# Kernel optimization log

Hardware: AMD Instinct MI355X
Metric: run time of the kernel (lower is better)

Reference implementation:

```python
import jax, jax.numpy as jnp
import numpy as np

# nuScenes-scale config: batch 2, 360x360 BEV grid (1440/4), 128 channels,
# 10 classes, 200 proposals, 3x3 NMS kernel, 40k occupied voxels per sample.
B, H, W_GRID, NUM_CLS, NUM_PROP, NMS_K = 2, 360, 360, 10, 200, 3
C = 128
N_PER_B = 40000
NEG_FILL = -1000000.0  # scatter_nd fill value from to_dense()


def _bev_pos():
    # replicates create_2D_grid: coord = (x_index_along_dim1, y_index_along_dim0)
    xs = jnp.arange(H, dtype=jnp.float32)
    ys = jnp.arange(W_GRID, dtype=jnp.float32)
    by, bx = jnp.meshgrid(xs, ys, indexing='ij')  # by[i,j]=i, bx[i,j]=j
    return jnp.stack([bx, by], axis=-1).reshape(-1, 2)  # [H*W, 2]


def setup_inputs() -> dict:
    key = jax.random.key(0)
    ks = jax.random.split(key, 10)
    # unique spatial locations per batch sample (sparse voxel coords)
    flats = [jax.random.permutation(ks[i], H * W_GRID)[:N_PER_B] for i in range(B)]
    flat = jnp.concatenate(flats)
    b = jnp.repeat(jnp.arange(B), N_PER_B)
    indices = jnp.stack([b, flat // W_GRID, flat % W_GRID], axis=1).astype(jnp.int32)
    features = jax.random.normal(ks[4], (B * N_PER_B, C), jnp.float32)
    # heatmap head (pointwise linears standing in for the submconv stack)
    W_hm1 = jax.random.normal(ks[5], (C, C), jnp.float32) * (2.0 / C) ** 0.5
    b_hm1 = jnp.zeros((C,), jnp.float32)
    W_hm2 = jax.random.normal(ks[6], (C, NUM_CLS), jnp.float32) * (2.0 / C) ** 0.5
    b_hm2 = jnp.full((NUM_CLS,), -2.19, jnp.float32)  # fc[-1].bias.fill_(-2.19)
    # class_encoding: nn.Conv1d(num_class, channels, 1)
    W_cls = jax.random.normal(ks[7], (C, NUM_CLS), jnp.float32) * 0.1
    b_cls = jnp.zeros((C,), jnp.float32)
    return dict(features=features, W_hm1=W_hm1, b_hm1=b_hm1, W_hm2=W_hm2,
                b_hm2=b_hm2, W_cls=W_cls, b_cls=b_cls, indices=indices)


def reference(features, W_hm1, b_hm1, W_hm2, b_hm2, W_cls, b_cls, indices):
    bidx, yi, xi = indices[:, 0], indices[:, 1], indices[:, 2]
    HW = H * W_GRID

    # --- x.dense(): scatter voxel features to dense BEV grid (zero fill) ---
    xd = jnp.zeros((B, H, W_GRID, C), features.dtype).at[bidx, yi, xi].set(features)
    x_flat = xd.reshape(B, HW, C).transpose(0, 2, 1)  # [B, C, HW]

    # --- heatmap head (per-voxel) then to_dense() with -1e6 fill ---
    hm = jax.nn.relu(features @ W_hm1 + b_hm1) @ W_hm2 + b_hm2  # [N, NUM_CLS]
    dense_hm = jnp.full((B, H, W_GRID, NUM_CLS), NEG_FILL, hm.dtype)
    dense_hm = dense_hm.at[bidx, yi, xi].set(hm).transpose(0, 3, 1, 2)  # [B,K,H,W]

    heat = jax.nn.sigmoid(dense_hm)  # detached in original

    # --- NMS-kernel peak extraction ---
    pad = NMS_K // 2
    inner = jax.lax.reduce_window(heat, -jnp.inf, jax.lax.max,
                                  (1, 1, NMS_K, NMS_K), (1, 1, 1, 1), 'VALID')
    local_max = jnp.zeros_like(heat).at[:, :, pad:H - pad, pad:W_GRID - pad].set(inner)
    # pedestrian (8) and traffic_cone (9): kernel size 1
    local_max = local_max.at[:, 8].set(heat[:, 8]).at[:, 9].set(heat[:, 9])
    heat = heat * (heat == local_max)
    heat_f = heat.reshape(B, NUM_CLS, HW)

    # --- top-k proposals over (class, location) ---
    _, top = jax.lax.top_k(heat_f.reshape(B, -1), NUM_PROP)  # [B, P]
    cls = top // HW
    idx = top % HW

    # --- gather proposal features + class encoding ---
    qf = jnp.take_along_axis(x_flat, jnp.broadcast_to(idx[:, None, :], (B, C, NUM_PROP)), axis=2)
    onehot = jax.nn.one_hot(cls, NUM_CLS, dtype=qf.dtype)  # [B, P, K]
    qf = qf + jnp.einsum('ck,bpk->bcp', W_cls, onehot) + b_cls[None, :, None]

    # --- proposal positions and heatmap scores ---
    query_pos = _bev_pos()[idx]  # [B, P, 2]
    qhs = jnp.take_along_axis(heat_f, jnp.broadcast_to(idx[:, None, :], (B, NUM_CLS, NUM_PROP)), axis=2)
    return qf, query_pos, qhs, cls
```

## Files before the change

### kernel.cpp

```cpp
#include <hip/hip_runtime.h>

#define HW 129600
#define WG 360
#define HG 360
#define NCLS 10
#define NPROP 200
#define CDIM 128
#define NROWS 80000
#define NB 2
#define NPB (NROWS / NB)
#define SEL_CAP 4096
#define HBINS 4096
#define RPB 64
#define PSTR 12

__device__ __forceinline__ void lds_cp16(float* l, const float* g) {
  __builtin_amdgcn_global_load_lds(
      (const __attribute__((address_space(1))) void*)g,
      (__attribute__((address_space(3))) void*)l, 16, 0, 0);
}

__device__ __forceinline__ float4 fmax4(float4 a, float4 b) {
  float4 r;
  r.x = fmaxf(a.x, b.x);
  r.y = fmaxf(a.y, b.y);
  r.z = fmaxf(a.z, b.z);
  r.w = fmaxf(a.w, b.w);
  return r;
}

__global__ __launch_bounds__(256) void k_head(
    const float* __restrict__ feat, const float* __restrict__ W1,
    const float* __restrict__ b1, const float* __restrict__ W2,
    const float* __restrict__ b2, const int* __restrict__ idxs,
    float* __restrict__ dense_heat, int* __restrict__ rowmap) {
  __shared__ __align__(16) float lds_w[2][32 * 128];
  __shared__ __align__(16) float lds_f[2][RPB * 32];
  __shared__ int lds_b[RPB];
  __shared__ int lds_p[RPB];
  const int tid = threadIdx.x;
  const int row0 = blockIdx.x * RPB;
  const int tc = tid & 31;
  const int tr = tid >> 5;
  const int wv = tid >> 6;
  const int lane = tid & 63;

  auto stage = [&](int kt, int nb) {
#pragma unroll
    for (int c = 0; c < 4; ++c) {
      const int off = (wv * 4 + c) * 256;
      lds_cp16(&lds_w[nb][off], W1 + kt * 4096 + off + lane * 4);
    }
#pragma unroll
    for (int c = 0; c < 2; ++c) {
      const int off = (wv * 2 + c) * 256;
      const int fidx = off + lane * 4;
      const int r = fidx >> 5, kk = fidx & 31;
      lds_cp16(&lds_f[nb][off],
               feat + (size_t)(row0 + r) * CDIM + kt * 32 + kk);
    }
  };

  stage(0, 0);
  if (tid < RPB) {
    int row = row0 + tid;
    int bb = idxs[row * 3 + 0];
    int yy = idxs[row * 3 + 1];
    int xx = idxs[row * 3 + 2];
    lds_b[tid] = bb;
    lds_p[tid] = yy * WG + xx;
    rowmap[(size_t)bb * HW + yy * WG + xx] = row;
  }
  __syncthreads();

  float acc[8][4];
#pragma unroll
  for (int r = 0; r < 8; ++r)
#pragma unroll
    for (int c = 0; c < 4; ++c) acc[r][c] = 0.f;

  for (int kt = 0; kt < 4; ++kt) {
    const int cb = kt & 1;
    if (kt < 3) stage(kt + 1, cb ^ 1);
#pragma unroll
    for (int kg = 0; kg < 8; ++kg) {
      float4 w0 = *(const float4*)(&lds_w[cb][(kg * 4 + 0) * 128 + tc * 4]);
      float4 w1 = *(const float4*)(&lds_w[cb][(kg * 4 + 1) * 128 + tc * 4]);
      float4 w2 = *(const float4*)(&lds_w[cb][(kg * 4 + 2) * 128 + tc * 4]);
      float4 w3 = *(const float4*)(&lds_w[cb][(kg * 4 + 3) * 128 + tc * 4]);
#pragma unroll
      for (int r = 0; r < 8; ++r) {
        float4 fv = *(const float4*)(&lds_f[cb][(tr * 8 + r) * 32 + kg * 4]);
        acc[r][0] = fmaf(fv.x, w0.x, acc[r][0]);
        acc[r][0] = fmaf(fv.y, w1.x, acc[r][0]);
        acc[r][0] = fmaf(fv.z, w2.x, acc[r][0]);
        acc[r][0] = fmaf(fv.w, w3.x, acc[r][0]);
        acc[r][1] = fmaf(fv.x, w0.y, acc[r][1]);
        acc[r][1] = fmaf(fv.y, w1.y, acc[r][1]);
        acc[r][1] = fmaf(fv.z, w2.y, acc[r][1]);
        acc[r][1] = fmaf(fv.w, w3.y, acc[r][1]);
        acc[r][2] = fmaf(fv.x, w0.z, acc[r][2]);
        acc[r][2] = fmaf(fv.y, w1.z, acc[r][2]);
        acc[r][2] = fmaf(fv.z, w2.z, acc[r][2]);
        acc[r][2] = fmaf(fv.w, w3.z, acc[r][2]);
        acc[r][3] = fmaf(fv.x, w0.w, acc[r][3]);
        acc[r][3] = fmaf(fv.y, w1.w, acc[r][3]);
        acc[r][3] = fmaf(fv.z, w2.w, acc[r][3]);
        acc[r][3] = fmaf(fv.w, w3.w, acc[r][3]);
      }
    }
    __syncthreads();
  }

  float* w2t = &lds_f[0][0];
  for (int i = tid; i < CDIM * NCLS; i += 256) {
    int k = i / NCLS, j = i - k * NCLS;
    w2t[j * 128 + k] = W2[i];
  }
  __syncthreads();

  float* hbuf = &lds_w[0][0];
  float4 b1v = *(const float4*)(b1 + tc * 4);
#pragma unroll
  for (int half = 0; half < 2; ++half) {
    if ((tr >> 2) == half) {
      int ltr = tr & 3;
#pragma unroll
      for (int r = 0; r < 8; ++r) {
        float4 h;
        h.x = fmaxf(acc[r][0] + b1v.x, 0.f);
        h.y = fmaxf(acc[r][1] + b1v.y, 0.f);
        h.z = fmaxf(acc[r][2] + b1v.z, 0.f);
        h.w = fmaxf(acc[r][3] + b1v.w, 0.f);
        *(float4*)(hbuf + (ltr * 8 + r) * 128 + tc * 4) = h;
      }
    }
    __syncthreads();
    for (int o = tid; o < 32 * NCLS; o += 256) {
      int r = o / NCLS, j = o - r * NCLS;
      float s = b2[j];
      for (int i4 = 0; i4 < 32; ++i4) {
        int k4 = (i4 + tid) & 31;
        float4 hv = *(const float4*)(hbuf + r * 128 + k4 * 4);
        float4 wv2 = *(const float4*)(w2t + j * 128 + k4 * 4);
        s = fmaf(hv.x, wv2.x, s);
        s = fmaf(hv.y, wv2.y, s);
        s = fmaf(hv.z, wv2.z, s);
        s = fmaf(hv.w, wv2.w, s);
      }
      float heat = 1.0f / (1.0f + expf(-s));
      int gr = half * 32 + r;
      dense_heat[((size_t)lds_b[gr] * HW + lds_p[gr]) * PSTR + j] = heat;
    }
    __syncthreads();
  }
}

__global__ __launch_bounds__(256) void k_hist(
    const float* __restrict__ dense_heat, const int* __restrict__ idxs,
    float* __restrict__ val, unsigned int* __restrict__ hist) {
  __shared__ unsigned int lh[HBINS];
  const int tid = threadIdx.x;
  const int row = blockIdx.x * 256 + tid;
  const int blk_b = (blockIdx.x * 256 >= NPB) ? 1 : 0;
  for (int i = tid; i < HBINS; i += 256) lh[i] = 0;
  __syncthreads();

  float v[10];
  int bb = 0;
  const bool valid = row < NROWS;
  if (valid) {
    bb = (row >= NPB) ? 1 : 0;
    const int y = idxs[row * 3 + 1];
    const int x = idxs[row * 3 + 2];
    const int pos = y * WG + x;
    const float* base = dense_heat + ((size_t)bb * HW + pos) * PSTR;
    const bool interior = (y > 0 && y < HG - 1 && x > 0 && x < WG - 1);
    const int d[8] = {-1, 1, -WG - 1, -WG, -WG + 1, WG - 1, WG, WG + 1};
#pragma unroll
    for (int g = 0; g < 2; ++g) {
      float4 cen = *(const float4*)(base + g * 4);
      if (interior) {
        float4 m = cen;
#pragma unroll
        for (int n = 0; n < 8; ++n)
          m = fmax4(m, *(const float4*)(base + d[n] * PSTR + g * 4));
        v[g * 4 + 0] = (cen.x == m.x) ? cen.x : 0.f;
        v[g * 4 + 1] = (cen.y == m.y) ? cen.y : 0.f;
        v[g * 4 + 2] = (cen.z == m.z) ? cen.z : 0.f;
        v[g * 4 + 3] = (cen.w == m.w) ? cen.w : 0.f;
      } else {
        v[g * 4 + 0] = v[g * 4 + 1] = v[g * 4 + 2] = v[g * 4 + 3] = 0.f;
      }
    }
    float2 c89 = *(const float2*)(base + 8);
    v[8] = c89.x;
    v[9] = c89.y;
    float4 s0 = {v[0], v[1], v[2], v[3]};
    float4 s1 = {v[4], v[5], v[6], v[7]};
    float4 s2 = {v[8], v[9], 0.f, 0.f};
    *(float4*)(val + (size_t)row * PSTR + 0) = s0;
    *(float4*)(val + (size_t)row * PSTR + 4) = s1;
    *(float4*)(val + (size_t)row * PSTR + 8) = s2;
#pragma unroll
    for (int c = 0; c < 10; ++c) {
      if (v[c] > 0.f) {
        unsigned int bin = __float_as_uint(v[c]) >> 18;
        if (bb == blk_b)
          atomicAdd(&lh[bin], 1u);
        else
          atomicAdd(&hist[(size_t)bb * HBINS + bin], 1u);
      }
    }
  }
  __syncthreads();
  unsigned int* gh = hist + (size_t)blk_b * HBINS;
  for (int i = tid; i < HBINS; i += 256) {
    unsigned int c = lh[i];
    if (c) atomicAdd(&gh[i], c);
  }
}

__global__ __launch_bounds__(256) void k_collect(
    const float* __restrict__ val, const int* __restrict__ idxs,
    const unsigned int* __restrict__ hist, unsigned long long* __restrict__ sel,
    int* __restrict__ sel_cnt) {
  __shared__ unsigned int coarse[256];
  __shared__ int sT[2];
  const int tid = threadIdx.x;
  for (int bb = 0; bb < NB; ++bb) {
    const unsigned int* h = hist + (size_t)bb * HBINS;
    unsigned int s = 0;
#pragma unroll
    for (int i = 0; i < HBINS / 256; ++i) s += h[tid * (HBINS / 256) + i];
    coarse[tid] = s;
    __syncthreads();
    if (tid == 0) {
      unsigned int cum = 0;
      int T = 0;
      int ci = 255;
      for (; ci >= 0; --ci) {
        if (cum + coarse[ci] >= NPROP) break;
        cum += coarse[ci];
      }
      if (ci >= 0) {
        int t = 15;
        for (; t > 0; --t) {
          unsigned int c = h[ci * 16 + t];
          if (cum + c >= NPROP) break;
          cum += c;
        }
        T = ci * 16 + t;
      }
      sT[bb] = T;
    }
    __syncthreads();
  }
  const int row = blockIdx.x * 256 + tid;
  const bool valid = row < NROWS;
  const int bb = (valid && row >= NPB) ? 1 : 0;
  const int T = sT[bb];
  float v[12];
  int pos = 0;
  if (valid) {
    *(float4*)(v + 0) = *(const float4*)(val + (size_t)row * PSTR + 0);
    *(float4*)(v + 4) = *(const float4*)(val + (size_t)row * PSTR + 4);
    *(float4*)(v + 8) = *(const float4*)(val + (size_t)row * PSTR + 8);
    pos = idxs[row * 3 + 1] * WG + idxs[row * 3 + 2];
  }
  const int lane = tid & 63;
#pragma unroll
  for (int cl = 0; cl < 10; ++cl) {
    float vv = valid ? v[cl] : 0.f;
    unsigned int bits = __float_as_uint(vv);
    bool pred = (vv > 0.f) && ((int)(bits >> 18) >= T);
    unsigned long long m0 = __ballot(pred && (bb == 0));
    unsigned long long m1 = __ballot(pred && (bb == 1));
    if (pred) {
      unsigned long long mask = bb ? m1 : m0;
      int leader = __ffsll((unsigned long long)mask) - 1;
      int lb = __popcll(mask & ((1ull << lane) - 1ull));
      int base = 0;
      if (lane == leader) base = atomicAdd(&sel_cnt[bb], (int)__popcll(mask));
      base = __shfl(base, leader, 64);
      unsigned int gidx = (unsigned int)cl * HW + (unsigned int)pos;
      unsigned long long key =
          ((unsigned long long)bits << 32) | (unsigned long long)(~gidx);
      int slot = base + lb;
      if (slot < SEL_CAP) sel[(size_t)bb * SEL_CAP + slot] = key;
    }
  }
}

__global__ __launch_bounds__(256) void k_final(
    const unsigned long long* __restrict__ sel, const int* __restrict__ sel_cnt,
    const float* __restrict__ val, const int* __restrict__ rowmap,
    const float* __restrict__ feat, const float* __restrict__ Wc,
    const float* __restrict__ bc, float* __restrict__ out) {
  __shared__ unsigned long long sk[SEL_CAP];
  __shared__ unsigned long long winners[NPROP];
  __shared__ int wcls[NPROP];
  __shared__ int wrow[NPROP];
  const int b = blockIdx.x;
  const int tid = threadIdx.x;
  int M = sel_cnt[b];
  if (M > SEL_CAP) M = SEL_CAP;
  for (int i = tid; i < M; i += 256) sk[i] = sel[(size_t)b * SEL_CAP + i];
  __syncthreads();
  for (int i = tid; i < M; i += 256) {
    unsigned long long key = sk[i];
    int rank = 0;
    for (int j = 0; j < M; ++j) rank += (sk[j] > key) ? 1 : 0;
    if (rank < NPROP) winners[rank] = key;
  }
  __syncthreads();
  if (tid < NPROP) {
    unsigned long long key = winners[tid];
    unsigned int gidx = ~((unsigned int)(key & 0xFFFFFFFFull));
    int cls = (int)(gidx / HW);
    int pos = (int)(gidx - (unsigned int)cls * HW);
    int y = pos / WG, x = pos - y * WG;
    wcls[tid] = cls;
    wrow[tid] = rowmap[(size_t)b * HW + pos];
    out[51200 + ((size_t)b * NPROP + tid) * 2 + 0] = (float)x;
    out[51200 + ((size_t)b * NPROP + tid) * 2 + 1] = (float)y;
    out[56000 + b * NPROP + tid] = (float)cls;
  }
  __syncthreads();
  for (int o = tid; o < NCLS * NPROP; o += 256) {
    int j = o / NPROP, pp = o - j * NPROP;
    out[52000 + (size_t)b * NCLS * NPROP + o] = val[(size_t)wrow[pp] * PSTR + j];
  }
  for (int o = tid; o < CDIM * NPROP; o += 256) {
    int c = o / NPROP, pp = o - c * NPROP;
    out[(size_t)b * CDIM * NPROP + o] =
        feat[(size_t)wrow[pp] * CDIM + c] + Wc[c * NCLS + wcls[pp]] + bc[c];
  }
}

extern "C" void kernel_launch(void* const* d_in, const int* in_sizes, int n_in,
                              void* d_out, int out_size, void* d_ws,
                              size_t ws_size, hipStream_t stream) {
  const float* feat = (const float*)d_in[0];
  const float* W1 = (const float*)d_in[1];
  const float* b1 = (const float*)d_in[2];
  const float* W2 = (const float*)d_in[3];
  const float* b2 = (const float*)d_in[4];
  const float* Wc = (const float*)d_in[5];
  const float* bc = (const float*)d_in[6];
  const int* idxs = (const int*)d_in[7];
  float* out = (float*)d_out;

  char* ws = (char*)d_ws;
  float* dense_heat = (float*)(ws + 0);
  unsigned int* hist = (unsigned int*)(ws + 12441600);
  int* rowmap = (int*)(ws + 12474368);
  unsigned long long* sel = (unsigned long long*)(ws + 13511168);
  int* sel_cnt = (int*)(ws + 13576704);
  float* val = (float*)(ws + 13576720);

  hipMemsetAsync(dense_heat, 0, (size_t)NB * HW * PSTR * sizeof(float), stream);
  hipMemsetAsync(hist, 0, (size_t)NB * HBINS * sizeof(unsigned int), stream);
  hipMemsetAsync(sel_cnt, 0, 2 * sizeof(int), stream);

  k_head<<<NROWS / RPB, 256, 0, stream>>>(feat, W1, b1, W2, b2, idxs, dense_heat,
                                          rowmap);
  k_hist<<<(NROWS + 255) / 256, 256, 0, stream>>>(dense_heat, idxs, val, hist);
  k_collect<<<(NROWS + 255) / 256, 256, 0, stream>>>(val, idxs, hist, sel,
                                                     sel_cnt);
  k_final<<<NB, 256, 0, stream>>>(sel, sel_cnt, val, rowmap, feat, Wc, bc, out);
}
```

Baseline: 202.7 us.

## Replace dense heat grid with compact per-row heat and fuse tail kernels

Stores sigmoid heat per voxel row instead of scattering it into a zeroed dense BEV grid. This removes the large memset and the dense writes. NMS neighbours are now found through the rowmap and validated against the indices, so stale rowmap entries are tolerated without a memset. Histogram, threshold, collect and final top-k are fused into one 256-block kernel that uses grid-wide atomic barriers. Clearing hist and counters moves into the head kernel. The persistent-grid spin barrier depends on all 256 blocks being co-resident, and the neighbour lookups add indirect gathers.

New measurement: 293.1 us. 1.45x slower.

```diff
diff --git a/kernel.cpp b/kernel.cpp
--- a/kernel.cpp
+++ b/kernel.cpp
@@ -13,6 +13,7 @@
 #define HBINS 4096
 #define RPB 64
 #define PSTR 12
+#define TBLK 256
 
 __device__ __forceinline__ void lds_cp16(float* l, const float* g) {
   __builtin_amdgcn_global_load_lds(
@@ -29,15 +30,68 @@
   return r;
 }
 
+__device__ __forceinline__ unsigned int ald_u32(const unsigned int* p) {
+  return __hip_atomic_load(p, __ATOMIC_RELAXED, __HIP_MEMORY_SCOPE_AGENT);
+}
+__device__ __forceinline__ unsigned long long ald_u64(
+    const unsigned long long* p) {
+  return __hip_atomic_load(p, __ATOMIC_RELAXED, __HIP_MEMORY_SCOPE_AGENT);
+}
+__device__ __forceinline__ void ast_u64(unsigned long long* p,
+                                        unsigned long long v) {
+  __hip_atomic_store(p, v, __ATOMIC_RELAXED, __HIP_MEMORY_SCOPE_AGENT);
+}
+
+__device__ __forceinline__ void nms_row(int bb, int y, int x, int row,
+                                        const int* __restrict__ rowmap,
+                                        const float* __restrict__ heat12,
+                                        const int* __restrict__ idxs,
+                                        float* vv) {
+  const float* ch = heat12 + (size_t)row * PSTR;
+  float4 c0 = *(const float4*)ch;
+  float4 c1 = *(const float4*)(ch + 4);
+  float2 c89 = *(const float2*)(ch + 8);
+  if (y > 0 && y < HG - 1 && x > 0 && x < WG - 1) {
+    float4 m0 = c0, m1 = c1;
+    const int dy[8] = {0, 0, -1, -1, -1, 1, 1, 1};
+    const int dx[8] = {-1, 1, -1, 0, 1, -1, 0, 1};
+#pragma unroll
+    for (int n = 0; n < 8; ++n) {
+      int ny = y + dy[n], nx = x + dx[n];
+      int nr = rowmap[(size_t)bb * HW + ny * WG + nx];
+      if ((unsigned)nr < NROWS) {
+        if (idxs[nr * 3 + 0] == bb && idxs[nr * 3 + 1] == ny &&
+            idxs[nr * 3 + 2] == nx) {
+          const float* nh = heat12 + (size_t)nr * PSTR;
+          m0 = fmax4(m0, *(const float4*)nh);
+          m1 = fmax4(m1, *(const float4*)(nh + 4));
+        }
+      }
+    }
+    vv[0] = (c0.x == m0.x) ? c0.x : 0.f;
+    vv[1] = (c0.y == m0.y) ? c0.y : 0.f;
+    vv[2] = (c0.z == m0.z) ? c0.z : 0.f;
+    vv[3] = (c0.w == m0.w) ? c0.w : 0.f;
+    vv[4] = (c1.x == m1.x) ? c1.x : 0.f;
+    vv[5] = (c1.y == m1.y) ? c1.y : 0.f;
+    vv[6] = (c1.z == m1.z) ? c1.z : 0.f;
+    vv[7] = (c1.w == m1.w) ? c1.w : 0.f;
+  } else {
+#pragma unroll
+    for (int c = 0; c < 8; ++c) vv[c] = 0.f;
+  }
+  vv[8] = c89.x;
+  vv[9] = c89.y;
+}
+
 __global__ __launch_bounds__(256) void k_head(
     const float* __restrict__ feat, const float* __restrict__ W1,
     const float* __restrict__ b1, const float* __restrict__ W2,
     const float* __restrict__ b2, const int* __restrict__ idxs,
-    float* __restrict__ dense_heat, int* __restrict__ rowmap) {
+    float* __restrict__ heat12, int* __restrict__ rowmap,
+    unsigned int* __restrict__ hist, int* __restrict__ cnts) {
   __shared__ __align__(16) float lds_w[2][32 * 128];
   __shared__ __align__(16) float lds_f[2][RPB * 32];
-  __shared__ int lds_b[RPB];
-  __shared__ int lds_p[RPB];
   const int tid = threadIdx.x;
   const int row0 = blockIdx.x * RPB;
   const int tc = tid & 31;
@@ -45,6 +99,9 @@
   const int wv = tid >> 6;
   const int lane = tid & 63;
 
+  if (blockIdx.x < 32) hist[blockIdx.x * 256 + tid] = 0;
+  if (blockIdx.x == 32 && tid < 4) cnts[tid] = 0;
+
   auto stage = [&](int kt, int nb) {
 #pragma unroll
     for (int c = 0; c < 4; ++c) {
@@ -67,8 +124,6 @@
     int bb = idxs[row * 3 + 0];
     int yy = idxs[row * 3 + 1];
     int xx = idxs[row * 3 + 2];
-    lds_b[tid] = bb;
-    lds_p[tid] = yy * WG + xx;
     rowmap[(size_t)bb * HW + yy * WG + xx] = row;
   }
   __syncthreads();
@@ -149,90 +204,74 @@
         s = fmaf(hv.w, wv2.w, s);
       }
       float heat = 1.0f / (1.0f + expf(-s));
-      int gr = half * 32 + r;
-      dense_heat[((size_t)lds_b[gr] * HW + lds_p[gr]) * PSTR + j] = heat;
+      heat12[(size_t)(row0 + half * 32 + r) * PSTR + j] = heat;
     }
     __syncthreads();
   }
 }
 
-__global__ __launch_bounds__(256) void k_hist(
-    const float* __restrict__ dense_heat, const int* __restrict__ idxs,
-    float* __restrict__ val, unsigned int* __restrict__ hist) {
-  __shared__ unsigned int lh[HBINS];
-  const int tid = threadIdx.x;
-  const int row = blockIdx.x * 256 + tid;
-  const int blk_b = (blockIdx.x * 256 >= NPB) ? 1 : 0;
-  for (int i = tid; i < HBINS; i += 256) lh[i] = 0;
-  __syncthreads();
-
-  float v[10];
-  int bb = 0;
-  const bool valid = row < NROWS;
-  if (valid) {
-    bb = (row >= NPB) ? 1 : 0;
-    const int y = idxs[row * 3 + 1];
-    const int x = idxs[row * 3 + 2];
-    const int pos = y * WG + x;
-    const float* base = dense_heat + ((size_t)bb * HW + pos) * PSTR;
-    const bool interior = (y > 0 && y < HG - 1 && x > 0 && x < WG - 1);
-    const int d[8] = {-1, 1, -WG - 1, -WG, -WG + 1, WG - 1, WG, WG + 1};
-#pragma unroll
-    for (int g = 0; g < 2; ++g) {
-      float4 cen = *(const float4*)(base + g * 4);
-      if (interior) {
-        float4 m = cen;
-#pragma unroll
-        for (int n = 0; n < 8; ++n)
-          m = fmax4(m, *(const float4*)(base + d[n] * PSTR + g * 4));
-        v[g * 4 + 0] = (cen.x == m.x) ? cen.x : 0.f;
-        v[g * 4 + 1] = (cen.y == m.y) ? cen.y : 0.f;
-        v[g * 4 + 2] = (cen.z == m.z) ? cen.z : 0.f;
-        v[g * 4 + 3] = (cen.w == m.w) ? cen.w : 0.f;
-      } else {
-        v[g * 4 + 0] = v[g * 4 + 1] = v[g * 4 + 2] = v[g * 4 + 3] = 0.f;
-      }
-    }
-    float2 c89 = *(const float2*)(base + 8);
-    v[8] = c89.x;
-    v[9] = c89.y;
-    float4 s0 = {v[0], v[1], v[2], v[3]};
-    float4 s1 = {v[4], v[5], v[6], v[7]};
-    float4 s2 = {v[8], v[9], 0.f, 0.f};
-    *(float4*)(val + (size_t)row * PSTR + 0) = s0;
-    *(float4*)(val + (size_t)row * PSTR + 4) = s1;
-    *(float4*)(val + (size_t)row * PSTR + 8) = s2;
-#pragma unroll
-    for (int c = 0; c < 10; ++c) {
-      if (v[c] > 0.f) {
-        unsigned int bin = __float_as_uint(v[c]) >> 18;
-        if (bb == blk_b)
-          atomicAdd(&lh[bin], 1u);
-        else
-          atomicAdd(&hist[(size_t)bb * HBINS + bin], 1u);
-      }
-    }
-  }
-  __syncthreads();
-  unsigned int* gh = hist + (size_t)blk_b * HBINS;
-  for (int i = tid; i < HBINS; i += 256) {
-    unsigned int c = lh[i];
-    if (c) atomicAdd(&gh[i], c);
-  }
-}
-
-__global__ __launch_bounds__(256) void k_collect(
-    const float* __restrict__ val, const int* __restrict__ idxs,
-    const unsigned int* __restrict__ hist, unsigned long long* __restrict__ sel,
-    int* __restrict__ sel_cnt) {
+__global__ __launch_bounds__(256) void k_tail(
+    const float* __restrict__ heat12, const int* __restrict__ rowmap,
+    const int* __restrict__ idxs, unsigned int* __restrict__ hist,
+    unsigned long long* __restrict__ sel, int* __restrict__ cnts,
+    const float* __restrict__ feat, const float* __restrict__ Wc,
+    const float* __restrict__ bc, float* __restrict__ out) {
+  __shared__ __align__(16) unsigned long long sk[SEL_CAP];
   __shared__ unsigned int coarse[256];
   __shared__ int sT[2];
+  __shared__ unsigned long long winners[NPROP];
+  __shared__ float wq[NPROP * NCLS];
+  __shared__ int wrow[NPROP];
+  __shared__ int wcls[NPROP];
+  unsigned int* lh = (unsigned int*)sk;
+  int* sel_cnt = cnts + 0;
+  int* done = cnts + 2;
   const int tid = threadIdx.x;
+  const int lane = tid & 63;
+
+  for (int i = tid; i < 2 * HBINS; i += 256) lh[i] = 0;
+  __syncthreads();
+  float vv[2][10];
+  int rw[2], ps[2], bbv[2];
+#pragma unroll
+  for (int s = 0; s < 2; ++s) {
+    int row = blockIdx.x * 256 + tid + s * 65536;
+    rw[s] = row;
+    if (row < NROWS) {
+      int bb = (row >= NPB) ? 1 : 0;
+      int y = idxs[row * 3 + 1];
+      int x = idxs[row * 3 + 2];
+      bbv[s] = bb;
+      ps[s] = y * WG + x;
+      nms_row(bb, y, x, row, rowmap, heat12, idxs, vv[s]);
+#pragma unroll
+      for (int c = 0; c < 10; ++c) {
+        if (vv[s][c] > 0.f)
+          atomicAdd(&lh[bb * HBINS + (__float_as_uint(vv[s][c]) >> 18)], 1u);
+      }
+    }
+  }
+  __syncthreads();
+  for (int i = tid; i < 2 * HBINS; i += 256) {
+    unsigned int c = lh[i];
+    if (c) atomicAdd(&hist[i], c);
+  }
+  __syncthreads();
+  __threadfence();
+  if (tid == 0) {
+    __hip_atomic_fetch_add(&done[0], 1, __ATOMIC_RELEASE,
+                           __HIP_MEMORY_SCOPE_AGENT);
+    while (__hip_atomic_load(&done[0], __ATOMIC_ACQUIRE,
+                             __HIP_MEMORY_SCOPE_AGENT) < TBLK)
+      __builtin_amdgcn_s_sleep(2);
+  }
+  __syncthreads();
+
   for (int bb = 0; bb < NB; ++bb) {
     const unsigned int* h = hist + (size_t)bb * HBINS;
     unsigned int s = 0;
 #pragma unroll
-    for (int i = 0; i < HBINS / 256; ++i) s += h[tid * (HBINS / 256) + i];
+    for (int i = 0; i < HBINS / 256; ++i) s += ald_u32(&h[tid * (HBINS / 256) + i]);
     coarse[tid] = s;
     __syncthreads();
     if (tid == 0) {
@@ -246,7 +285,7 @@
       if (ci >= 0) {
         int t = 15;
         for (; t > 0; --t) {
-          unsigned int c = h[ci * 16 + t];
+          unsigned int c = ald_u32(&h[ci * 16 + t]);
           if (cum + c >= NPROP) break;
           cum += c;
         }
@@ -256,56 +295,51 @@
     }
     __syncthreads();
   }
-  const int row = blockIdx.x * 256 + tid;
-  const bool valid = row < NROWS;
-  const int bb = (valid && row >= NPB) ? 1 : 0;
-  const int T = sT[bb];
-  float v[12];
-  int pos = 0;
-  if (valid) {
-    *(float4*)(v + 0) = *(const float4*)(val + (size_t)row * PSTR + 0);
-    *(float4*)(v + 4) = *(const float4*)(val + (size_t)row * PSTR + 4);
-    *(float4*)(v + 8) = *(const float4*)(val + (size_t)row * PSTR + 8);
-    pos = idxs[row * 3 + 1] * WG + idxs[row * 3 + 2];
-  }
-  const int lane = tid & 63;
-#pragma unroll
-  for (int cl = 0; cl < 10; ++cl) {
-    float vv = valid ? v[cl] : 0.f;
-    unsigned int bits = __float_as_uint(vv);
-    bool pred = (vv > 0.f) && ((int)(bits >> 18) >= T);
-    unsigned long long m0 = __ballot(pred && (bb == 0));
-    unsigned long long m1 = __ballot(pred && (bb == 1));
-    if (pred) {
-      unsigned long long mask = bb ? m1 : m0;
-      int leader = __ffsll((unsigned long long)mask) - 1;
-      int lb = __popcll(mask & ((1ull << lane) - 1ull));
-      int base = 0;
-      if (lane == leader) base = atomicAdd(&sel_cnt[bb], (int)__popcll(mask));
-      base = __shfl(base, leader, 64);
-      unsigned int gidx = (unsigned int)cl * HW + (unsigned int)pos;
-      unsigned long long key =
-          ((unsigned long long)bits << 32) | (unsigned long long)(~gidx);
-      int slot = base + lb;
-      if (slot < SEL_CAP) sel[(size_t)bb * SEL_CAP + slot] = key;
-    }
-  }
-}
-
-__global__ __launch_bounds__(256) void k_final(
-    const unsigned long long* __restrict__ sel, const int* __restrict__ sel_cnt,
-    const float* __restrict__ val, const int* __restrict__ rowmap,
-    const float* __restrict__ feat, const float* __restrict__ Wc,
-    const float* __restrict__ bc, float* __restrict__ out) {
-  __shared__ unsigned long long sk[SEL_CAP];
-  __shared__ unsigned long long winners[NPROP];
-  __shared__ int wcls[NPROP];
-  __shared__ int wrow[NPROP];
+#pragma unroll
+  for (int s = 0; s < 2; ++s) {
+    bool rowok = rw[s] < NROWS;
+    int bb = rowok ? bbv[s] : 0;
+    int T = sT[bb];
+#pragma unroll
+    for (int cl = 0; cl < 10; ++cl) {
+      float v = rowok ? vv[s][cl] : 0.f;
+      unsigned int bits = __float_as_uint(v);
+      bool pred = (v > 0.f) && ((int)(bits >> 18) >= T);
+      unsigned long long m0 = __ballot(pred && (bb == 0));
+      unsigned long long m1 = __ballot(pred && (bb == 1));
+      if (pred) {
+        unsigned long long mask = bb ? m1 : m0;
+        int leader = __ffsll((unsigned long long)mask) - 1;
+        int lb = __popcll(mask & ((1ull << lane) - 1ull));
+        int base = 0;
+        if (lane == leader) base = atomicAdd(&sel_cnt[bb], (int)__popcll(mask));
+        base = __shfl(base, leader, 64);
+        unsigned int gidx = (unsigned int)cl * HW + (unsigned int)ps[s];
+        unsigned long long key =
+            ((unsigned long long)bits << 32) | (unsigned long long)(~gidx);
+        int slot = base + lb;
+        if (slot < SEL_CAP) ast_u64(&sel[(size_t)bb * SEL_CAP + slot], key);
+      }
+    }
+  }
+  __syncthreads();
+  __threadfence();
+  if (tid == 0)
+    __hip_atomic_fetch_add(&done[1], 1, __ATOMIC_RELEASE,
+                           __HIP_MEMORY_SCOPE_AGENT);
+  if (blockIdx.x >= NB) return;
+  if (tid == 0) {
+    while (__hip_atomic_load(&done[1], __ATOMIC_ACQUIRE,
+                             __HIP_MEMORY_SCOPE_AGENT) < TBLK)
+      __builtin_amdgcn_s_sleep(2);
+  }
+  __syncthreads();
+
   const int b = blockIdx.x;
-  const int tid = threadIdx.x;
-  int M = sel_cnt[b];
+  int M = __hip_atomic_load(&sel_cnt[b], __ATOMIC_RELAXED,
+                            __HIP_MEMORY_SCOPE_AGENT);
   if (M > SEL_CAP) M = SEL_CAP;
-  for (int i = tid; i < M; i += 256) sk[i] = sel[(size_t)b * SEL_CAP + i];
+  for (int i = tid; i < M; i += 256) sk[i] = ald_u64(&sel[(size_t)b * SEL_CAP + i]);
   __syncthreads();
   for (int i = tid; i < M; i += 256) {
     unsigned long long key = sk[i];
@@ -320,16 +354,21 @@
     int cls = (int)(gidx / HW);
     int pos = (int)(gidx - (unsigned int)cls * HW);
     int y = pos / WG, x = pos - y * WG;
+    int row = rowmap[(size_t)b * HW + pos];
+    wrow[tid] = row;
     wcls[tid] = cls;
-    wrow[tid] = rowmap[(size_t)b * HW + pos];
     out[51200 + ((size_t)b * NPROP + tid) * 2 + 0] = (float)x;
     out[51200 + ((size_t)b * NPROP + tid) * 2 + 1] = (float)y;
     out[56000 + b * NPROP + tid] = (float)cls;
+    float q[10];
+    nms_row(b, y, x, row, rowmap, heat12, idxs, q);
+#pragma unroll
+    for (int j = 0; j < NCLS; ++j) wq[tid * NCLS + j] = q[j];
   }
   __syncthreads();
   for (int o = tid; o < NCLS * NPROP; o += 256) {
     int j = o / NPROP, pp = o - j * NPROP;
-    out[52000 + (size_t)b * NCLS * NPROP + o] = val[(size_t)wrow[pp] * PSTR + j];
+    out[52000 + (size_t)b * NCLS * NPROP + o] = wq[pp * NCLS + j];
   }
   for (int o = tid; o < CDIM * NPROP; o += 256) {
     int c = o / NPROP, pp = o - c * NPROP;
@@ -352,21 +391,14 @@
   float* out = (float*)d_out;
 
   char* ws = (char*)d_ws;
-  float* dense_heat = (float*)(ws + 0);
-  unsigned int* hist = (unsigned int*)(ws + 12441600);
-  int* rowmap = (int*)(ws + 12474368);
-  unsigned long long* sel = (unsigned long long*)(ws + 13511168);
-  int* sel_cnt = (int*)(ws + 13576704);
-  float* val = (float*)(ws + 13576720);
-
-  hipMemsetAsync(dense_heat, 0, (size_t)NB * HW * PSTR * sizeof(float), stream);
-  hipMemsetAsync(hist, 0, (size_t)NB * HBINS * sizeof(unsigned int), stream);
-  hipMemsetAsync(sel_cnt, 0, 2 * sizeof(int), stream);
-
-  k_head<<<NROWS / RPB, 256, 0, stream>>>(feat, W1, b1, W2, b2, idxs, dense_heat,
-                                          rowmap);
-  k_hist<<<(NROWS + 255) / 256, 256, 0, stream>>>(dense_heat, idxs, val, hist);
-  k_collect<<<(NROWS + 255) / 256, 256, 0, stream>>>(val, idxs, hist, sel,
-                                                     sel_cnt);
-  k_final<<<NB, 256, 0, stream>>>(sel, sel_cnt, val, rowmap, feat, Wc, bc, out);
-}
+  float* heat12 = (float*)(ws + 0);
+  int* rowmap = (int*)(ws + 3840000);
+  unsigned int* hist = (unsigned int*)(ws + 4876800);
+  unsigned long long* sel = (unsigned long long*)(ws + 4909568);
+  int* cnts = (int*)(ws + 4975104);
+
+  k_head<<<NROWS / RPB, 256, 0, stream>>>(feat, W1, b1, W2, b2, idxs, heat12,
+                                          rowmap, hist, cnts);
+  k_tail<<<TBLK, 256, 0, stream>>>(heat12, rowmap, idxs, hist, sel, cnts, feat,
+                                   Wc, bc, out);
+}
```
